# Kernel tuning notes

Measured on AMD Instinct MI355X. Metric: run time of the kernel, lower is better.

Reference implementation:

```python
import jax, jax.numpy as jnp
import numpy as np

N = 50000
E = 800000
C_IN, C_HID, C_OUT = 512, 128, 2
HEADS2 = 3
NEG_SLOPE = 0.2


def gat_conv(x, src, dst, W, att_src, att_dst, bias, heads, ch, concat):
    """PyG GATConv (eval mode) on pre-augmented (self-loop included) edge lists.
    x: [N, F_in], W: [F_in, heads*ch], att_*: [heads, ch], bias: [heads*ch] or [ch].
    """
    n = x.shape[0]
    h = (x @ W).reshape(n, heads, ch)                 # [N, H, C]
    a_src = (h * att_src).sum(-1)                     # [N, H]
    a_dst = (h * att_dst).sum(-1)                     # [N, H]
    e = jax.nn.leaky_relu(a_src[src] + a_dst[dst], NEG_SLOPE)  # [E', H]
    # segment softmax over edges sharing a destination node
    m = jax.ops.segment_max(e, dst, num_segments=n)
    m = jnp.where(jnp.isfinite(m), m, 0.0)
    ex = jnp.exp(e - m[dst])
    denom = jax.ops.segment_sum(ex, dst, num_segments=n)
    alpha = ex / (denom[dst] + 1e-16)                 # [E', H]
    out = jax.ops.segment_sum(h[src] * alpha[:, :, None], dst, num_segments=n)  # [N, H, C]
    out = out.reshape(n, heads * ch) if concat else out.mean(axis=1)
    return out + bias


def setup_inputs() -> dict:
    key = jax.random.key(0)
    ks = jax.random.split(key, 12)
    x = jax.random.normal(ks[0], (N, C_IN), dtype=jnp.float32)
    edge_index = jax.random.randint(ks[1], (2, E), 0, N, dtype=jnp.int64)
    s1 = 1.0 / np.sqrt(C_IN)
    s2 = 1.0 / np.sqrt(C_HID)
    return {
        "x": x,
        "edge_index": edge_index,
        "W1": jax.random.normal(ks[2], (C_IN, C_HID), dtype=jnp.float32) * s1,
        "att_src1": jax.random.normal(ks[3], (1, C_HID), dtype=jnp.float32) * s2,
        "att_dst1": jax.random.normal(ks[4], (1, C_HID), dtype=jnp.float32) * s2,
        "bias1": jnp.zeros((C_HID,), dtype=jnp.float32),
        "W2": jax.random.normal(ks[5], (C_HID, HEADS2 * C_OUT), dtype=jnp.float32) * s2,
        "att_src2": jax.random.normal(ks[6], (HEADS2, C_OUT), dtype=jnp.float32) * 0.5,
        "att_dst2": jax.random.normal(ks[7], (HEADS2, C_OUT), dtype=jnp.float32) * 0.5,
        "bias2": jnp.zeros((C_OUT,), dtype=jnp.float32),
    }


def reference(x, edge_index, W1, att_src1, att_dst1, bias1, W2, att_src2, att_dst2, bias2):
    n = x.shape[0]
    loop = jnp.arange(n, dtype=edge_index.dtype)
    src = jnp.concatenate([edge_index[0], loop])      # PyG add_self_loops=True
    dst = jnp.concatenate([edge_index[1], loop])
    h = gat_conv(x, src, dst, W1, att_src1, att_dst1, bias1, 1, C_HID, True)
    h = jax.nn.relu(h)                                # Dropout is identity in eval
    out = gat_conv(h, src, dst, W2, att_src2, att_dst2, bias2, HEADS2, C_OUT, False)
    return out
```

## Files before the change

kernel.cpp:

```cpp
#include <hip/hip_runtime.h>

#define N_NODES 50000
#define N_EDGES 800000
#define E_TOT   850000
#define C_IN    512
#define C_HID   128
#define NEG     0.2f

typedef _Float16 f16x8 __attribute__((ext_vector_type(8)));
typedef __attribute__((ext_vector_type(4))) float f32x4;

__device__ __forceinline__ float leaky(float x) { return x > 0.f ? x : NEG * x; }

union U32H2 { unsigned u; _Float16 h[2]; float f; };
union BFrag { uint4 u; f16x8 h; };

__device__ __forceinline__ unsigned short f2h(float f) {
  U32H2 c; c.h[0] = (_Float16)f; return (unsigned short)(c.u & 0xffff);
}

__device__ __forceinline__ unsigned pk2h(float a, float b) {
  union { __fp16 v __attribute__((ext_vector_type(2))); unsigned u; } c;
  c.v = __builtin_amdgcn_cvt_pkrtz(a, b);
  return c.u;
}

__global__ __launch_bounds__(256) void prep_v_kernel(const float* __restrict__ W1,
    const float* __restrict__ as1, const float* __restrict__ ad1,
    float* __restrict__ v1s, float* __restrict__ v1d) {
  const int wv = threadIdx.x >> 6, lane = threadIdx.x & 63;
  const int k = blockIdx.x * 4 + wv;
  if (k >= C_IN) return;
  float2 w = *(const float2*)(W1 + (size_t)k * C_HID + 2 * lane);
  float2 a = *(const float2*)(as1 + 2 * lane);
  float2 d = *(const float2*)(ad1 + 2 * lane);
  float s = w.x * a.x + w.y * a.y;
  float t = w.x * d.x + w.y * d.y;
#pragma unroll
  for (int m = 32; m >= 1; m >>= 1) {
    s += __shfl_xor(s, m, 64);
    t += __shfl_xor(t, m, 64);
  }
  if (lane == 0) { v1s[k] = s; v1d[k] = t; }
}

__global__ __launch_bounds__(256) void prep_w_kernel(const float* __restrict__ W1,
    unsigned short* __restrict__ Wswz) {
  int t = blockIdx.x * 256 + threadIdx.x;
  int c = t >> 6, kc = t & 63;
  if (c >= C_HID) return;
  int kblk = kc >> 2, q = kc & 3;
  int ct = c >> 4, l15 = c & 15;
  int lane = q * 16 + l15;
  unsigned short hb[8], lb[8];
#pragma unroll
  for (int i = 0; i < 8; i++) {
    float w = W1[(size_t)(kc * 8 + i) * C_HID + c];
    _Float16 hi = (_Float16)w;
    _Float16 lo = (_Float16)(w - (float)hi);
    U32H2 ch; ch.h[0] = hi;
    U32H2 cl; cl.h[0] = lo;
    hb[i] = (unsigned short)(ch.u & 0xffff);
    lb[i] = (unsigned short)(cl.u & 0xffff);
  }
  size_t chunk0 = ((size_t)(kblk * 8 + ct) * 2) * 512;
  *(uint4*)&Wswz[chunk0 + (size_t)lane * 8]       = *(uint4*)hb;
  *(uint4*)&Wswz[chunk0 + 512 + (size_t)lane * 8] = *(uint4*)lb;
}

__global__ __launch_bounds__(256) void lin1_kernel(const float* __restrict__ x,
    const unsigned short* __restrict__ Wswz,
    const float* __restrict__ v1s, const float* __restrict__ v1d,
    unsigned short* __restrict__ h1u, float* __restrict__ a_src, float* __restrict__ a_dst) {
  __shared__ __attribute__((aligned(16))) unsigned short As[64][40];

  const int tid  = threadIdx.x;
  const int lane = tid & 63, wv = tid >> 6;
  const int m0   = blockIdx.x * 64;

  const int arow = tid >> 2, kseg = (tid & 3) * 8;
  int grow = m0 + arow;
  if (grow >= N_NODES) grow = N_NODES - 1;
  const float* xrow = x + (size_t)grow * C_IN + kseg;

  f32x4 acc[4][2];
#pragma unroll
  for (int rt = 0; rt < 4; rt++) { acc[rt][0] = (f32x4)0.f; acc[rt][1] = (f32x4)0.f; }
  float ps = 0.f, pd = 0.f;

  const int q = lane >> 4, l15 = lane & 15;

  float4 xa = *(const float4*)(xrow);
  float4 xb = *(const float4*)(xrow + 4);

  for (int kblk = 0; kblk < 16; kblk++) {
    const int k0 = kblk * 32;
    float4 vsa = *(const float4*)(v1s + k0 + kseg);
    float4 vsb = *(const float4*)(v1s + k0 + kseg + 4);
    float4 vda = *(const float4*)(v1d + k0 + kseg);
    float4 vdb = *(const float4*)(v1d + k0 + kseg + 4);
    ps += xa.x * vsa.x + xa.y * vsa.y + xa.z * vsa.z + xa.w * vsa.w
        + xb.x * vsb.x + xb.y * vsb.y + xb.z * vsb.z + xb.w * vsb.w;
    pd += xa.x * vda.x + xa.y * vda.y + xa.z * vda.z + xa.w * vda.w
        + xb.x * vdb.x + xb.y * vdb.y + xb.z * vdb.z + xb.w * vdb.w;
    uint4 pk = make_uint4(pk2h(xa.x, xa.y), pk2h(xa.z, xa.w),
                          pk2h(xb.x, xb.y), pk2h(xb.z, xb.w));

    __syncthreads();
    *(uint4*)&As[arow][kseg] = pk;
    if (kblk < 15) {
      xa = *(const float4*)(xrow + k0 + 32);
      xb = *(const float4*)(xrow + k0 + 36);
    }
    __syncthreads();

    const unsigned short* bp = Wswz + ((size_t)(kblk * 8 + wv * 2) * 2) * 512 + (size_t)lane * 8;
    BFrag b00, b01, b10, b11;
    b00.u = *(const uint4*)(bp);
    b01.u = *(const uint4*)(bp + 512);
    b10.u = *(const uint4*)(bp + 1024);
    b11.u = *(const uint4*)(bp + 1536);

#pragma unroll
    for (int rt = 0; rt < 4; rt++) {
      f16x8 af = *(const f16x8*)&As[rt * 16 + l15][q * 8];
      acc[rt][0] = __builtin_amdgcn_mfma_f32_16x16x32_f16(af, b00.h, acc[rt][0], 0, 0, 0);
      acc[rt][0] = __builtin_amdgcn_mfma_f32_16x16x32_f16(af, b01.h, acc[rt][0], 0, 0, 0);
      acc[rt][1] = __builtin_amdgcn_mfma_f32_16x16x32_f16(af, b10.h, acc[rt][1], 0, 0, 0);
      acc[rt][1] = __builtin_amdgcn_mfma_f32_16x16x32_f16(af, b11.h, acc[rt][1], 0, 0, 0);
    }
  }

  ps += __shfl_xor(ps, 1, 64); ps += __shfl_xor(ps, 2, 64);
  pd += __shfl_xor(pd, 1, 64); pd += __shfl_xor(pd, 2, 64);
  if ((tid & 3) == 0) {
    int row = m0 + arow;
    if (row < N_NODES) { a_src[row] = ps; a_dst[row] = pd; }
  }

#pragma unroll
  for (int rt = 0; rt < 4; rt++) {
    int rbase = m0 + rt * 16 + q * 4;
#pragma unroll
    for (int ct = 0; ct < 2; ct++) {
      int col = wv * 32 + ct * 16 + l15;
#pragma unroll
      for (int ri = 0; ri < 4; ri++) {
        int row = rbase + ri;
        if (row < N_NODES)
          h1u[(size_t)row * C_HID + col] = f2h(acc[rt][ct][ri]);
      }
    }
  }
}

__global__ void deg_kernel(const int* __restrict__ ei, int* __restrict__ deg) {
  int e = blockIdx.x * blockDim.x + threadIdx.x;
  if (e >= N_EDGES) return;
  atomicAdd(&deg[ei[N_EDGES + e]], 1);
}

__global__ __launch_bounds__(1024) void scan_kernel(const int* __restrict__ deg,
                                                    int* __restrict__ rowptr,
                                                    int* __restrict__ cursor) {
  __shared__ int wsum[16];
  const int tid = threadIdx.x, lane = tid & 63, wv = tid >> 6;
  int carry = 0;
  for (int base = 0; base < N_NODES; base += 8192) {
    int i0 = base + tid * 8;
    int v[8];
    if (i0 + 8 <= N_NODES) {
      int4 va = *(const int4*)(deg + i0);
      int4 vb = *(const int4*)(deg + i0 + 4);
      v[0]=va.x+1; v[1]=va.y+1; v[2]=va.z+1; v[3]=va.w+1;
      v[4]=vb.x+1; v[5]=vb.y+1; v[6]=vb.z+1; v[7]=vb.w+1;
    } else {
#pragma unroll
      for (int i = 0; i < 8; i++) v[i] = (i0 + i < N_NODES) ? deg[i0 + i] + 1 : 0;
    }
    int tsum = 0;
#pragma unroll
    for (int i = 0; i < 8; i++) tsum += v[i];
    int sc = tsum;
#pragma unroll
    for (int off = 1; off < 64; off <<= 1) {
      int t = __shfl_up(sc, off, 64);
      if (lane >= off) sc += t;
    }
    if (lane == 63) wsum[wv] = sc;
    __syncthreads();
    if (wv == 0 && lane < 16) {
      int s = wsum[lane];
#pragma unroll
      for (int off = 1; off < 16; off <<= 1) {
        int t = __shfl_up(s, off, 64);
        if (lane >= off) s += t;
      }
      wsum[lane] = s;
    }
    __syncthreads();
    int ex = carry + (wv ? wsum[wv - 1] : 0) + sc - tsum;
#pragma unroll
    for (int i = 0; i < 8; i++) {
      if (i0 + i < N_NODES) { rowptr[i0 + i] = ex; cursor[i0 + i] = ex; }
      ex += v[i];
    }
    carry += wsum[15];
    __syncthreads();
  }
  if (tid == 0) rowptr[N_NODES] = carry;
}

__global__ void bucket_kernel(const int* __restrict__ ei, int* __restrict__ cursor,
                              const float* __restrict__ a_src, const float* __restrict__ a_dst,
                              int2* __restrict__ esw) {
  int e = blockIdx.x * blockDim.x + threadIdx.x;
  if (e >= E_TOT) return;
  int src, dst;
  if (e < N_EDGES) { src = ei[e]; dst = ei[N_EDGES + e]; }
  else             { src = dst = e - N_EDGES; }
  float w = __expf(leaky(a_src[src] + a_dst[dst]));
  int slot = atomicAdd(&cursor[dst], 1);
  U32H2 c; c.f = w;
  esw[slot] = make_int2(src, (int)c.u);
}

__global__ __launch_bounds__(256) void agg1_kernel(const unsigned short* __restrict__ h1u,
    const int2* __restrict__ esw, const int* __restrict__ rowptr,
    const float* __restrict__ bias1, const float* __restrict__ W2,
    const float* __restrict__ as2w, const float* __restrict__ ad2w,
    float* __restrict__ h2, float* __restrict__ as2, float* __restrict__ ad2) {
  const int wv = threadIdx.x >> 6, lane = threadIdx.x & 63;
  const int q = lane >> 4, r = lane & 15;
  const int n = blockIdx.x * 4 + wv;
  if (n >= N_NODES) return;
  const int start = rowptr[n], end = rowptr[n + 1];

  float acc[8];
#pragma unroll
  for (int i = 0; i < 8; i++) acc[i] = 0.f;
  float wsum = 0.f;

  const unsigned short* hbase = h1u + r * 8;

  for (int base = start; base < end; base += 64) {
    int idx = base + lane;
    int sreg = 0; float wreg = 0.f;
    if (idx < end) {
      int2 sv = esw[idx];
      sreg = sv.x;
      U32H2 c; c.u = (unsigned)sv.y;
      wreg = c.f;
    }
    wsum += wreg;
    const int cnt = min(64, end - base);
    const int nit = (cnt + 7) >> 3;
    for (int i = 0; i < nit; i++) {
      int e0 = 8 * i + q, e1 = 8 * i + 4 + q;
      int   s0 = __shfl(sreg, e0, 64);
      int   s1 = __shfl(sreg, e1, 64);
      float w0 = __shfl(wreg, e0, 64);
      float w1 = __shfl(wreg, e1, 64);
      uint4 g0 = *(const uint4*)(hbase + (size_t)s0 * C_HID);
      uint4 g1 = *(const uint4*)(hbase + (size_t)s1 * C_HID);
      U32H2 c0, c1, c2, c3;
      c0.u = g0.x; c1.u = g0.y; c2.u = g0.z; c3.u = g0.w;
      acc[0] = fmaf(w0, (float)c0.h[0], acc[0]); acc[1] = fmaf(w0, (float)c0.h[1], acc[1]);
      acc[2] = fmaf(w0, (float)c1.h[0], acc[2]); acc[3] = fmaf(w0, (float)c1.h[1], acc[3]);
      acc[4] = fmaf(w0, (float)c2.h[0], acc[4]); acc[5] = fmaf(w0, (float)c2.h[1], acc[5]);
      acc[6] = fmaf(w0, (float)c3.h[0], acc[6]); acc[7] = fmaf(w0, (float)c3.h[1], acc[7]);
      c0.u = g1.x; c1.u = g1.y; c2.u = g1.z; c3.u = g1.w;
      acc[0] = fmaf(w1, (float)c0.h[0], acc[0]); acc[1] = fmaf(w1, (float)c0.h[1], acc[1]);
      acc[2] = fmaf(w1, (float)c1.h[0], acc[2]); acc[3] = fmaf(w1, (float)c1.h[1], acc[3]);
      acc[4] = fmaf(w1, (float)c2.h[0], acc[4]); acc[5] = fmaf(w1, (float)c2.h[1], acc[5]);
      acc[6] = fmaf(w1, (float)c3.h[0], acc[6]); acc[7] = fmaf(w1, (float)c3.h[1], acc[7]);
    }
  }

#pragma unroll
  for (int i = 0; i < 8; i++) {
    acc[i] += __shfl_xor(acc[i], 16, 64);
    acc[i] += __shfl_xor(acc[i], 32, 64);
  }
#pragma unroll
  for (int m = 32; m >= 1; m >>= 1) wsum += __shfl_xor(wsum, m, 64);
  const float inv = 1.f / wsum;

  float4 ba = *(const float4*)(bias1 + r * 8);
  float4 bb = *(const float4*)(bias1 + r * 8 + 4);
  float u[8] = {fmaxf(acc[0] * inv + ba.x, 0.f), fmaxf(acc[1] * inv + ba.y, 0.f),
                fmaxf(acc[2] * inv + ba.z, 0.f), fmaxf(acc[3] * inv + ba.w, 0.f),
                fmaxf(acc[4] * inv + bb.x, 0.f), fmaxf(acc[5] * inv + bb.y, 0.f),
                fmaxf(acc[6] * inv + bb.z, 0.f), fmaxf(acc[7] * inv + bb.w, 0.f)};
  float p[6] = {0, 0, 0, 0, 0, 0};
#pragma unroll
  for (int i = 0; i < 8; i++) {
    const float* w2r = W2 + (size_t)(r * 8 + i) * 6;
#pragma unroll
    for (int o = 0; o < 6; o++) p[o] = fmaf(u[i], w2r[o], p[o]);
  }
#pragma unroll
  for (int o = 0; o < 6; o++) {
#pragma unroll
    for (int msk = 8; msk >= 1; msk >>= 1) p[o] += __shfl_xor(p[o], msk, 64);
  }

  if (lane == 0) {
#pragma unroll
    for (int o = 0; o < 6; o++) h2[(size_t)n * 8 + o] = p[o];
#pragma unroll
    for (int h = 0; h < 3; h++) {
      as2[n * 4 + h] = p[2 * h] * as2w[2 * h] + p[2 * h + 1] * as2w[2 * h + 1];
      ad2[n * 4 + h] = p[2 * h] * ad2w[2 * h] + p[2 * h + 1] * ad2w[2 * h + 1];
    }
  }
}

__global__ __launch_bounds__(256) void agg2_kernel(const float* __restrict__ h2,
    const float* __restrict__ as2, const float* __restrict__ ad2,
    const int* __restrict__ rowptr, const int2* __restrict__ esw,
    const float* __restrict__ bias2, float* __restrict__ out) {
  const int wv = threadIdx.x >> 6, lane = threadIdx.x & 63;
  const int q = lane >> 4, r = lane & 15;
  const int n = blockIdx.x * 16 + wv * 4 + q;
  if (n >= N_NODES) return;
  const int start = rowptr[n], end = rowptr[n + 1];
  const float4 adv = *(const float4*)(ad2 + (size_t)n * 4);

  float d0 = 0.f, d1 = 0.f, d2 = 0.f;
  float a0 = 0.f, a1 = 0.f, a2 = 0.f, a3 = 0.f, a4 = 0.f, a5 = 0.f;
  for (int j = start + r; j < end; j += 16) {
    int s = esw[j].x;
    float4 asv = *(const float4*)(as2 + (size_t)s * 4);
    float4 hlo = *(const float4*)(h2 + (size_t)s * 8);
    float2 hhi = *(const float2*)(h2 + (size_t)s * 8 + 4);
    float e0 = __expf(leaky(asv.x + adv.x));
    float e1 = __expf(leaky(asv.y + adv.y));
    float e2 = __expf(leaky(asv.z + adv.z));
    d0 += e0; d1 += e1; d2 += e2;
    a0 += e0 * hlo.x; a1 += e0 * hlo.y;
    a2 += e1 * hlo.z; a3 += e1 * hlo.w;
    a4 += e2 * hhi.x; a5 += e2 * hhi.y;
  }
#pragma unroll
  for (int m = 8; m >= 1; m >>= 1) {
    d0 += __shfl_xor(d0, m, 64); d1 += __shfl_xor(d1, m, 64); d2 += __shfl_xor(d2, m, 64);
    a0 += __shfl_xor(a0, m, 64); a1 += __shfl_xor(a1, m, 64); a2 += __shfl_xor(a2, m, 64);
    a3 += __shfl_xor(a3, m, 64); a4 += __shfl_xor(a4, m, 64); a5 += __shfl_xor(a5, m, 64);
  }
  if (r == 0) {
    float o0 = (a0 / d0 + a2 / d1 + a4 / d2) * (1.f / 3.f) + bias2[0];
    float o1 = (a1 / d0 + a3 / d1 + a5 / d2) * (1.f / 3.f) + bias2[1];
    *(float2*)(out + (size_t)n * 2) = make_float2(o0, o1);
  }
}

extern "C" void kernel_launch(void* const* d_in, const int* in_sizes, int n_in,
                              void* d_out, int out_size, void* d_ws, size_t ws_size,
                              hipStream_t stream) {
  const float* x        = (const float*)d_in[0];
  const int*   ei       = (const int*)d_in[1];
  const float* W1       = (const float*)d_in[2];
  const float* att_src1 = (const float*)d_in[3];
  const float* att_dst1 = (const float*)d_in[4];
  const float* bias1    = (const float*)d_in[5];
  const float* W2       = (const float*)d_in[6];
  const float* att_src2 = (const float*)d_in[7];
  const float* att_dst2 = (const float*)d_in[8];
  const float* bias2    = (const float*)d_in[9];
  float* out = (float*)d_out;

  char* w = (char*)d_ws;
  auto alloc = [&](size_t bytes) {
    char* p = w;
    w += (bytes + 255) & ~(size_t)255;
    return p;
  };
  unsigned short* h1u    = (unsigned short*)alloc((size_t)N_NODES * C_HID * 2);
  unsigned short* Wswz   = (unsigned short*)alloc((size_t)C_IN * C_HID * 2 * 2);
  float*          v1s    = (float*)alloc((size_t)C_IN * 4);
  float*          v1d    = (float*)alloc((size_t)C_IN * 4);
  float*          a_src1 = (float*)alloc((size_t)N_NODES * 4);
  float*          a_dst1 = (float*)alloc((size_t)N_NODES * 4);
  int*            deg    = (int*)alloc((size_t)N_NODES * 4);
  int*            rowptr = (int*)alloc((size_t)(N_NODES + 4) * 4);
  int*            cursor = (int*)alloc((size_t)N_NODES * 4);
  int2*           esw    = (int2*)alloc((size_t)E_TOT * 8);
  float*          h2     = (float*)alloc((size_t)N_NODES * 8 * 4);
  float*          as2    = (float*)alloc((size_t)N_NODES * 4 * 4);
  float*          ad2    = (float*)alloc((size_t)N_NODES * 4 * 4);

  (void)hipMemsetAsync(deg, 0, (size_t)N_NODES * 4, stream);

  prep_v_kernel<<<C_IN / 4, 256, 0, stream>>>(W1, att_src1, att_dst1, v1s, v1d);
  prep_w_kernel<<<32, 256, 0, stream>>>(W1, Wswz);
  deg_kernel<<<(N_EDGES + 255) / 256, 256, 0, stream>>>(ei, deg);
  scan_kernel<<<1, 1024, 0, stream>>>(deg, rowptr, cursor);
  lin1_kernel<<<(N_NODES + 63) / 64, 256, 0, stream>>>(x, Wswz, v1s, v1d,
                                                       h1u, a_src1, a_dst1);
  bucket_kernel<<<(E_TOT + 255) / 256, 256, 0, stream>>>(ei, cursor, a_src1, a_dst1, esw);
  agg1_kernel<<<(N_NODES + 3) / 4, 256, 0, stream>>>(h1u, esw, rowptr, bias1, W2,
                                                     att_src2, att_dst2, h2, as2, ad2);
  agg2_kernel<<<(N_NODES + 15) / 16, 256, 0, stream>>>(h2, as2, ad2, rowptr, esw, bias2, out);
}
```

Measured before the change: 354.1 us.

## Fuse setup kernels, rank edges in degree pass, double-buffer lin1, pack layer-2 records

Merges the W1 swizzle, attention-vector prep and degree counting into one launch. The degree atomics now record each edge's rank, so bucketing becomes deterministic with no second atomic pass or cursor array. lin1 double-buffers its shared A tile to drop one barrier per k-step. agg1 preloads W2 into registers and gathers four neighbours per step, and agg2 reads one packed 12-float record per node instead of three separate arrays. The cost is an extra rank array that must be written and read, plus more registers in agg1.

```diff
diff --git a/kernel.cpp b/kernel.cpp
--- a/kernel.cpp
+++ b/kernel.cpp
@@ -25,54 +25,59 @@
   return c.u;
 }
 
-__global__ __launch_bounds__(256) void prep_v_kernel(const float* __restrict__ W1,
-    const float* __restrict__ as1, const float* __restrict__ ad1,
-    float* __restrict__ v1s, float* __restrict__ v1d) {
-  const int wv = threadIdx.x >> 6, lane = threadIdx.x & 63;
-  const int k = blockIdx.x * 4 + wv;
-  if (k >= C_IN) return;
-  float2 w = *(const float2*)(W1 + (size_t)k * C_HID + 2 * lane);
-  float2 a = *(const float2*)(as1 + 2 * lane);
-  float2 d = *(const float2*)(ad1 + 2 * lane);
-  float s = w.x * a.x + w.y * a.y;
-  float t = w.x * d.x + w.y * d.y;
-#pragma unroll
-  for (int m = 32; m >= 1; m >>= 1) {
-    s += __shfl_xor(s, m, 64);
-    t += __shfl_xor(t, m, 64);
-  }
-  if (lane == 0) { v1s[k] = s; v1d[k] = t; }
-}
-
-__global__ __launch_bounds__(256) void prep_w_kernel(const float* __restrict__ W1,
-    unsigned short* __restrict__ Wswz) {
-  int t = blockIdx.x * 256 + threadIdx.x;
-  int c = t >> 6, kc = t & 63;
-  if (c >= C_HID) return;
-  int kblk = kc >> 2, q = kc & 3;
-  int ct = c >> 4, l15 = c & 15;
-  int lane = q * 16 + l15;
-  unsigned short hb[8], lb[8];
-#pragma unroll
-  for (int i = 0; i < 8; i++) {
-    float w = W1[(size_t)(kc * 8 + i) * C_HID + c];
-    _Float16 hi = (_Float16)w;
-    _Float16 lo = (_Float16)(w - (float)hi);
-    U32H2 ch; ch.h[0] = hi;
-    U32H2 cl; cl.h[0] = lo;
-    hb[i] = (unsigned short)(ch.u & 0xffff);
-    lb[i] = (unsigned short)(cl.u & 0xffff);
-  }
-  size_t chunk0 = ((size_t)(kblk * 8 + ct) * 2) * 512;
-  *(uint4*)&Wswz[chunk0 + (size_t)lane * 8]       = *(uint4*)hb;
-  *(uint4*)&Wswz[chunk0 + 512 + (size_t)lane * 8] = *(uint4*)lb;
+__global__ __launch_bounds__(256) void setup_kernel(
+    const float* __restrict__ W1, const float* __restrict__ as1,
+    const float* __restrict__ ad1, const int* __restrict__ ei,
+    unsigned short* __restrict__ Wswz, float* __restrict__ v1s, float* __restrict__ v1d,
+    int* __restrict__ deg, int* __restrict__ rnk) {
+  const int b = blockIdx.x;
+  if (b < 32) {
+    int t = b * 256 + threadIdx.x;
+    int c = t >> 6, kc = t & 63;
+    if (c >= C_HID) return;
+    int kblk = kc >> 2, q = kc & 3;
+    int ct = c >> 4, l15 = c & 15;
+    int lane = q * 16 + l15;
+    unsigned short hb[8], lb[8];
+#pragma unroll
+    for (int i = 0; i < 8; i++) {
+      float w = W1[(size_t)(kc * 8 + i) * C_HID + c];
+      _Float16 hi = (_Float16)w;
+      _Float16 lo = (_Float16)(w - (float)hi);
+      U32H2 ch; ch.h[0] = hi;
+      U32H2 cl; cl.h[0] = lo;
+      hb[i] = (unsigned short)(ch.u & 0xffff);
+      lb[i] = (unsigned short)(cl.u & 0xffff);
+    }
+    size_t chunk0 = ((size_t)(kblk * 8 + ct) * 2) * 512;
+    *(uint4*)&Wswz[chunk0 + (size_t)lane * 8]       = *(uint4*)hb;
+    *(uint4*)&Wswz[chunk0 + 512 + (size_t)lane * 8] = *(uint4*)lb;
+  } else if (b < 160) {
+    const int wv = threadIdx.x >> 6, lane = threadIdx.x & 63;
+    const int k = (b - 32) * 4 + wv;
+    if (k >= C_IN) return;
+    float2 w = *(const float2*)(W1 + (size_t)k * C_HID + 2 * lane);
+    float2 a = *(const float2*)(as1 + 2 * lane);
+    float2 d = *(const float2*)(ad1 + 2 * lane);
+    float s = w.x * a.x + w.y * a.y;
+    float t = w.x * d.x + w.y * d.y;
+#pragma unroll
+    for (int m = 32; m >= 1; m >>= 1) {
+      s += __shfl_xor(s, m, 64);
+      t += __shfl_xor(t, m, 64);
+    }
+    if (lane == 0) { v1s[k] = s; v1d[k] = t; }
+  } else {
+    int e = (b - 160) * 256 + threadIdx.x;
+    if (e < N_EDGES) rnk[e] = atomicAdd(&deg[ei[N_EDGES + e]], 1);
+  }
 }
 
 __global__ __launch_bounds__(256) void lin1_kernel(const float* __restrict__ x,
     const unsigned short* __restrict__ Wswz,
     const float* __restrict__ v1s, const float* __restrict__ v1d,
     unsigned short* __restrict__ h1u, float* __restrict__ a_src, float* __restrict__ a_dst) {
-  __shared__ __attribute__((aligned(16))) unsigned short As[64][40];
+  __shared__ __attribute__((aligned(16))) unsigned short As[2][64][40];
 
   const int tid  = threadIdx.x;
   const int lane = tid & 63, wv = tid >> 6;
@@ -93,8 +98,10 @@
   float4 xa = *(const float4*)(xrow);
   float4 xb = *(const float4*)(xrow + 4);
 
+#pragma unroll
   for (int kblk = 0; kblk < 16; kblk++) {
     const int k0 = kblk * 32;
+    const int buf = kblk & 1;
     float4 vsa = *(const float4*)(v1s + k0 + kseg);
     float4 vsb = *(const float4*)(v1s + k0 + kseg + 4);
     float4 vda = *(const float4*)(v1d + k0 + kseg);
@@ -103,16 +110,13 @@
         + xb.x * vsb.x + xb.y * vsb.y + xb.z * vsb.z + xb.w * vsb.w;
     pd += xa.x * vda.x + xa.y * vda.y + xa.z * vda.z + xa.w * vda.w
         + xb.x * vdb.x + xb.y * vdb.y + xb.z * vdb.z + xb.w * vdb.w;
-    uint4 pk = make_uint4(pk2h(xa.x, xa.y), pk2h(xa.z, xa.w),
-                          pk2h(xb.x, xb.y), pk2h(xb.z, xb.w));
-
+    *(uint4*)&As[buf][arow][kseg] = make_uint4(pk2h(xa.x, xa.y), pk2h(xa.z, xa.w),
+                                               pk2h(xb.x, xb.y), pk2h(xb.z, xb.w));
     __syncthreads();
-    *(uint4*)&As[arow][kseg] = pk;
     if (kblk < 15) {
       xa = *(const float4*)(xrow + k0 + 32);
       xb = *(const float4*)(xrow + k0 + 36);
     }
-    __syncthreads();
 
     const unsigned short* bp = Wswz + ((size_t)(kblk * 8 + wv * 2) * 2) * 512 + (size_t)lane * 8;
     BFrag b00, b01, b10, b11;
@@ -123,7 +127,7 @@
 
 #pragma unroll
     for (int rt = 0; rt < 4; rt++) {
-      f16x8 af = *(const f16x8*)&As[rt * 16 + l15][q * 8];
+      f16x8 af = *(const f16x8*)&As[buf][rt * 16 + l15][q * 8];
       acc[rt][0] = __builtin_amdgcn_mfma_f32_16x16x32_f16(af, b00.h, acc[rt][0], 0, 0, 0);
       acc[rt][0] = __builtin_amdgcn_mfma_f32_16x16x32_f16(af, b01.h, acc[rt][0], 0, 0, 0);
       acc[rt][1] = __builtin_amdgcn_mfma_f32_16x16x32_f16(af, b10.h, acc[rt][1], 0, 0, 0);
@@ -154,15 +158,8 @@
   }
 }
 
-__global__ void deg_kernel(const int* __restrict__ ei, int* __restrict__ deg) {
-  int e = blockIdx.x * blockDim.x + threadIdx.x;
-  if (e >= N_EDGES) return;
-  atomicAdd(&deg[ei[N_EDGES + e]], 1);
-}
-
 __global__ __launch_bounds__(1024) void scan_kernel(const int* __restrict__ deg,
-                                                    int* __restrict__ rowptr,
-                                                    int* __restrict__ cursor) {
+                                                    int* __restrict__ rowptr) {
   __shared__ int wsum[16];
   const int tid = threadIdx.x, lane = tid & 63, wv = tid >> 6;
   int carry = 0;
@@ -202,7 +199,7 @@
     int ex = carry + (wv ? wsum[wv - 1] : 0) + sc - tsum;
 #pragma unroll
     for (int i = 0; i < 8; i++) {
-      if (i0 + i < N_NODES) { rowptr[i0 + i] = ex; cursor[i0 + i] = ex; }
+      if (i0 + i < N_NODES) rowptr[i0 + i] = ex;
       ex += v[i];
     }
     carry += wsum[15];
@@ -211,38 +208,51 @@
   if (tid == 0) rowptr[N_NODES] = carry;
 }
 
-__global__ void bucket_kernel(const int* __restrict__ ei, int* __restrict__ cursor,
+__global__ void bucket_kernel(const int* __restrict__ ei, const int* __restrict__ rnk,
+                              const int* __restrict__ rowptr,
                               const float* __restrict__ a_src, const float* __restrict__ a_dst,
                               int2* __restrict__ esw) {
   int e = blockIdx.x * blockDim.x + threadIdx.x;
   if (e >= E_TOT) return;
-  int src, dst;
-  if (e < N_EDGES) { src = ei[e]; dst = ei[N_EDGES + e]; }
-  else             { src = dst = e - N_EDGES; }
-  float w = __expf(leaky(a_src[src] + a_dst[dst]));
-  int slot = atomicAdd(&cursor[dst], 1);
-  U32H2 c; c.f = w;
-  esw[slot] = make_int2(src, (int)c.u);
+  int src, slot;
+  if (e < N_EDGES) {
+    src = ei[e];
+    int dst = ei[N_EDGES + e];
+    slot = rowptr[dst] + rnk[e];
+    U32H2 c; c.f = __expf(leaky(a_src[src] + a_dst[dst]));
+    esw[slot] = make_int2(src, (int)c.u);
+  } else {
+    int n = e - N_EDGES;
+    slot = rowptr[n + 1] - 1;
+    U32H2 c; c.f = __expf(leaky(a_src[n] + a_dst[n]));
+    esw[slot] = make_int2(n, (int)c.u);
+  }
 }
 
 __global__ __launch_bounds__(256) void agg1_kernel(const unsigned short* __restrict__ h1u,
     const int2* __restrict__ esw, const int* __restrict__ rowptr,
     const float* __restrict__ bias1, const float* __restrict__ W2,
     const float* __restrict__ as2w, const float* __restrict__ ad2w,
-    float* __restrict__ h2, float* __restrict__ as2, float* __restrict__ ad2) {
+    float* __restrict__ hs2) {
   const int wv = threadIdx.x >> 6, lane = threadIdx.x & 63;
   const int q = lane >> 4, r = lane & 15;
   const int n = blockIdx.x * 4 + wv;
-  if (n >= N_NODES) return;
   const int start = rowptr[n], end = rowptr[n + 1];
 
-  float acc[8];
-#pragma unroll
-  for (int i = 0; i < 8; i++) acc[i] = 0.f;
+  float w2reg[8][6];
+#pragma unroll
+  for (int j = 0; j < 8; j++) {
+    const float* w2r = W2 + (size_t)(r * 8 + j) * 6;
+#pragma unroll
+    for (int o = 0; o < 6; o++) w2reg[j][o] = w2r[o];
+  }
+  float4 ba = *(const float4*)(bias1 + r * 8);
+  float4 bb = *(const float4*)(bias1 + r * 8 + 4);
+
+  const unsigned short* hbase = h1u + r * 8;
+
+  float acc[8] = {0, 0, 0, 0, 0, 0, 0, 0};
   float wsum = 0.f;
-
-  const unsigned short* hbase = h1u + r * 8;
-
   for (int base = start; base < end; base += 64) {
     int idx = base + lane;
     int sreg = 0; float wreg = 0.f;
@@ -254,26 +264,30 @@
     }
     wsum += wreg;
     const int cnt = min(64, end - base);
-    const int nit = (cnt + 7) >> 3;
-    for (int i = 0; i < nit; i++) {
-      int e0 = 8 * i + q, e1 = 8 * i + 4 + q;
-      int   s0 = __shfl(sreg, e0, 64);
-      int   s1 = __shfl(sreg, e1, 64);
-      float w0 = __shfl(wreg, e0, 64);
-      float w1 = __shfl(wreg, e1, 64);
+#pragma unroll
+    for (int i = 0; i < 4; i++) {
+      if (i * 16 >= cnt) break;
+      int   s0 = __shfl(sreg, i * 16 + q, 64);
+      int   s1 = __shfl(sreg, i * 16 + 4 + q, 64);
+      int   s2 = __shfl(sreg, i * 16 + 8 + q, 64);
+      int   s3 = __shfl(sreg, i * 16 + 12 + q, 64);
+      float w0 = __shfl(wreg, i * 16 + q, 64);
+      float w1 = __shfl(wreg, i * 16 + 4 + q, 64);
+      float w2 = __shfl(wreg, i * 16 + 8 + q, 64);
+      float w3 = __shfl(wreg, i * 16 + 12 + q, 64);
       uint4 g0 = *(const uint4*)(hbase + (size_t)s0 * C_HID);
       uint4 g1 = *(const uint4*)(hbase + (size_t)s1 * C_HID);
+      uint4 g2 = *(const uint4*)(hbase + (size_t)s2 * C_HID);
+      uint4 g3 = *(const uint4*)(hbase + (size_t)s3 * C_HID);
       U32H2 c0, c1, c2, c3;
-      c0.u = g0.x; c1.u = g0.y; c2.u = g0.z; c3.u = g0.w;
-      acc[0] = fmaf(w0, (float)c0.h[0], acc[0]); acc[1] = fmaf(w0, (float)c0.h[1], acc[1]);
-      acc[2] = fmaf(w0, (float)c1.h[0], acc[2]); acc[3] = fmaf(w0, (float)c1.h[1], acc[3]);
-      acc[4] = fmaf(w0, (float)c2.h[0], acc[4]); acc[5] = fmaf(w0, (float)c2.h[1], acc[5]);
-      acc[6] = fmaf(w0, (float)c3.h[0], acc[6]); acc[7] = fmaf(w0, (float)c3.h[1], acc[7]);
-      c0.u = g1.x; c1.u = g1.y; c2.u = g1.z; c3.u = g1.w;
-      acc[0] = fmaf(w1, (float)c0.h[0], acc[0]); acc[1] = fmaf(w1, (float)c0.h[1], acc[1]);
-      acc[2] = fmaf(w1, (float)c1.h[0], acc[2]); acc[3] = fmaf(w1, (float)c1.h[1], acc[3]);
-      acc[4] = fmaf(w1, (float)c2.h[0], acc[4]); acc[5] = fmaf(w1, (float)c2.h[1], acc[5]);
-      acc[6] = fmaf(w1, (float)c3.h[0], acc[6]); acc[7] = fmaf(w1, (float)c3.h[1], acc[7]);
+#define ACC8(G, W) \
+      c0.u = G.x; c1.u = G.y; c2.u = G.z; c3.u = G.w; \
+      acc[0] = fmaf(W, (float)c0.h[0], acc[0]); acc[1] = fmaf(W, (float)c0.h[1], acc[1]); \
+      acc[2] = fmaf(W, (float)c1.h[0], acc[2]); acc[3] = fmaf(W, (float)c1.h[1], acc[3]); \
+      acc[4] = fmaf(W, (float)c2.h[0], acc[4]); acc[5] = fmaf(W, (float)c2.h[1], acc[5]); \
+      acc[6] = fmaf(W, (float)c3.h[0], acc[6]); acc[7] = fmaf(W, (float)c3.h[1], acc[7]);
+      ACC8(g0, w0) ACC8(g1, w1) ACC8(g2, w2) ACC8(g3, w3)
+#undef ACC8
     }
   }
 
@@ -286,38 +300,38 @@
   for (int m = 32; m >= 1; m >>= 1) wsum += __shfl_xor(wsum, m, 64);
   const float inv = 1.f / wsum;
 
-  float4 ba = *(const float4*)(bias1 + r * 8);
-  float4 bb = *(const float4*)(bias1 + r * 8 + 4);
   float u[8] = {fmaxf(acc[0] * inv + ba.x, 0.f), fmaxf(acc[1] * inv + ba.y, 0.f),
                 fmaxf(acc[2] * inv + ba.z, 0.f), fmaxf(acc[3] * inv + ba.w, 0.f),
                 fmaxf(acc[4] * inv + bb.x, 0.f), fmaxf(acc[5] * inv + bb.y, 0.f),
                 fmaxf(acc[6] * inv + bb.z, 0.f), fmaxf(acc[7] * inv + bb.w, 0.f)};
   float p[6] = {0, 0, 0, 0, 0, 0};
 #pragma unroll
-  for (int i = 0; i < 8; i++) {
-    const float* w2r = W2 + (size_t)(r * 8 + i) * 6;
-#pragma unroll
-    for (int o = 0; o < 6; o++) p[o] = fmaf(u[i], w2r[o], p[o]);
-  }
+  for (int j = 0; j < 8; j++)
+#pragma unroll
+    for (int o = 0; o < 6; o++) p[o] = fmaf(u[j], w2reg[j][o], p[o]);
 #pragma unroll
   for (int o = 0; o < 6; o++) {
-#pragma unroll
-    for (int msk = 8; msk >= 1; msk >>= 1) p[o] += __shfl_xor(p[o], msk, 64);
+    p[o] += __shfl_xor(p[o], 1, 64);
+    p[o] += __shfl_xor(p[o], 2, 64);
+    p[o] += __shfl_xor(p[o], 4, 64);
+    p[o] += __shfl_xor(p[o], 8, 64);
   }
 
   if (lane == 0) {
-#pragma unroll
-    for (int o = 0; o < 6; o++) h2[(size_t)n * 8 + o] = p[o];
-#pragma unroll
-    for (int h = 0; h < 3; h++) {
-      as2[n * 4 + h] = p[2 * h] * as2w[2 * h] + p[2 * h + 1] * as2w[2 * h + 1];
-      ad2[n * 4 + h] = p[2 * h] * ad2w[2 * h] + p[2 * h + 1] * ad2w[2 * h + 1];
-    }
-  }
-}
-
-__global__ __launch_bounds__(256) void agg2_kernel(const float* __restrict__ h2,
-    const float* __restrict__ as2, const float* __restrict__ ad2,
+    float as0 = p[0] * as2w[0] + p[1] * as2w[1];
+    float as1 = p[2] * as2w[2] + p[3] * as2w[3];
+    float as2_ = p[4] * as2w[4] + p[5] * as2w[5];
+    float ad0 = p[0] * ad2w[0] + p[1] * ad2w[1];
+    float ad1 = p[2] * ad2w[2] + p[3] * ad2w[3];
+    float ad2_ = p[4] * ad2w[4] + p[5] * ad2w[5];
+    float* dst = hs2 + (size_t)n * 12;
+    *(float4*)(dst)     = make_float4(p[0], p[1], p[2], p[3]);
+    *(float4*)(dst + 4) = make_float4(p[4], p[5], as0, as1);
+    *(float4*)(dst + 8) = make_float4(as2_, ad0, ad1, ad2_);
+  }
+}
+
+__global__ __launch_bounds__(256) void agg2_kernel(const float* __restrict__ hs2,
     const int* __restrict__ rowptr, const int2* __restrict__ esw,
     const float* __restrict__ bias2, float* __restrict__ out) {
   const int wv = threadIdx.x >> 6, lane = threadIdx.x & 63;
@@ -325,22 +339,24 @@
   const int n = blockIdx.x * 16 + wv * 4 + q;
   if (n >= N_NODES) return;
   const int start = rowptr[n], end = rowptr[n + 1];
-  const float4 adv = *(const float4*)(ad2 + (size_t)n * 4);
+  float4 own = *(const float4*)(hs2 + (size_t)n * 12 + 8);
+  const float ad0 = own.y, ad1 = own.z, ad2 = own.w;
 
   float d0 = 0.f, d1 = 0.f, d2 = 0.f;
   float a0 = 0.f, a1 = 0.f, a2 = 0.f, a3 = 0.f, a4 = 0.f, a5 = 0.f;
   for (int j = start + r; j < end; j += 16) {
     int s = esw[j].x;
-    float4 asv = *(const float4*)(as2 + (size_t)s * 4);
-    float4 hlo = *(const float4*)(h2 + (size_t)s * 8);
-    float2 hhi = *(const float2*)(h2 + (size_t)s * 8 + 4);
-    float e0 = __expf(leaky(asv.x + adv.x));
-    float e1 = __expf(leaky(asv.y + adv.y));
-    float e2 = __expf(leaky(asv.z + adv.z));
+    const float* rec = hs2 + (size_t)s * 12;
+    float4 A = *(const float4*)(rec);
+    float4 B = *(const float4*)(rec + 4);
+    float  C = rec[8];
+    float e0 = __expf(leaky(B.z + ad0));
+    float e1 = __expf(leaky(B.w + ad1));
+    float e2 = __expf(leaky(C + ad2));
     d0 += e0; d1 += e1; d2 += e2;
-    a0 += e0 * hlo.x; a1 += e0 * hlo.y;
-    a2 += e1 * hlo.z; a3 += e1 * hlo.w;
-    a4 += e2 * hhi.x; a5 += e2 * hhi.y;
+    a0 += e0 * A.x; a1 += e0 * A.y;
+    a2 += e1 * A.z; a3 += e1 * A.w;
+    a4 += e2 * B.x; a5 += e2 * B.y;
   }
 #pragma unroll
   for (int m = 8; m >= 1; m >>= 1) {
@@ -384,22 +400,20 @@
   float*          a_dst1 = (float*)alloc((size_t)N_NODES * 4);
   int*            deg    = (int*)alloc((size_t)N_NODES * 4);
   int*            rowptr = (int*)alloc((size_t)(N_NODES + 4) * 4);
-  int*            cursor = (int*)alloc((size_t)N_NODES * 4);
+  int*            rnk    = (int*)alloc((size_t)N_EDGES * 4);
   int2*           esw    = (int2*)alloc((size_t)E_TOT * 8);
-  float*          h2     = (float*)alloc((size_t)N_NODES * 8 * 4);
-  float*          as2    = (float*)alloc((size_t)N_NODES * 4 * 4);
-  float*          ad2    = (float*)alloc((size_t)N_NODES * 4 * 4);
+  float*          hs2    = (float*)alloc((size_t)N_NODES * 12 * 4);
 
   (void)hipMemsetAsync(deg, 0, (size_t)N_NODES * 4, stream);
 
-  prep_v_kernel<<<C_IN / 4, 256, 0, stream>>>(W1, att_src1, att_dst1, v1s, v1d);
-  prep_w_kernel<<<32, 256, 0, stream>>>(W1, Wswz);
-  deg_kernel<<<(N_EDGES + 255) / 256, 256, 0, stream>>>(ei, deg);
-  scan_kernel<<<1, 1024, 0, stream>>>(deg, rowptr, cursor);
+  setup_kernel<<<160 + (N_EDGES + 255) / 256, 256, 0, stream>>>(
+      W1, att_src1, att_dst1, ei, Wswz, v1s, v1d, deg, rnk);
+  scan_kernel<<<1, 1024, 0, stream>>>(deg, rowptr);
   lin1_kernel<<<(N_NODES + 63) / 64, 256, 0, stream>>>(x, Wswz, v1s, v1d,
                                                        h1u, a_src1, a_dst1);
-  bucket_kernel<<<(E_TOT + 255) / 256, 256, 0, stream>>>(ei, cursor, a_src1, a_dst1, esw);
-  agg1_kernel<<<(N_NODES + 3) / 4, 256, 0, stream>>>(h1u, esw, rowptr, bias1, W2,
-                                                     att_src2, att_dst2, h2, as2, ad2);
-  agg2_kernel<<<(N_NODES + 15) / 16, 256, 0, stream>>>(h2, as2, ad2, rowptr, esw, bias2, out);
-}
+  bucket_kernel<<<(E_TOT + 255) / 256, 256, 0, stream>>>(ei, rnk, rowptr,
+                                                         a_src1, a_dst1, esw);
+  agg1_kernel<<<N_NODES / 4, 256, 0, stream>>>(h1u, esw, rowptr, bias1, W2,
+                                               att_src2, att_dst2, hs2);
+  agg2_kernel<<<(N_NODES + 15) / 16, 256, 0, stream>>>(hs2, rowptr, esw, bias2, out);
+}
```

Result: faster. 328.6 us (-7.2%).
